# Optimization experiments

Measured on AMD Instinct MI355X. Metric: run time of the kernel, lower is better.

The kernel has to match this reference:

```python
import jax, jax.numpy as jnp
import numpy as np

LN_EPS = 1e-5

def _layer_norm(y, g, b):
    mu = y.mean(-1, keepdims=True)
    var = y.var(-1, keepdims=True)
    return (y - mu) * jax.lax.rsqrt(var + LN_EPS) * g + b

def setup_inputs() -> dict:
    key = jax.random.key(0)
    ks = jax.random.split(key, 10)
    F, D, H = 32, 128, 128
    FD = F * D
    B = 8192
    def rn(k, shape, fan_in):
        return jax.random.normal(k, shape, dtype=jnp.float32) / np.sqrt(fan_in)
    return {
        "x":   jax.random.normal(ks[0], (B, F), dtype=jnp.float32),
        "Wp":  rn(ks[1], (F, D), 1), "bp": jnp.zeros((F, D), jnp.float32),
        "fW1": rn(ks[2], (F, D, H), D), "fb1": jnp.zeros((F, H), jnp.float32),
        "fW2": rn(ks[3], (F, H, D), H), "fb2": jnp.zeros((F, D), jnp.float32),
        "fWg": rn(ks[4], (F, D, 2 * D), D), "fbg": jnp.zeros((F, 2 * D), jnp.float32),
        "fg":  jnp.ones((F, D), jnp.float32), "fbe": jnp.zeros((F, D), jnp.float32),
        "sW1": rn(ks[5], (FD, H), FD), "sb1": jnp.zeros((H,), jnp.float32),
        "sW2": rn(ks[6], (H, FD), H), "sb2": jnp.zeros((FD,), jnp.float32),
        "sWg": rn(ks[7], (FD, 2 * FD), FD), "sbg": jnp.zeros((2 * FD,), jnp.float32),
        "sg":  jnp.ones((FD,), jnp.float32), "sbe": jnp.zeros((FD,), jnp.float32),
        "Wh":  rn(ks[8], (FD, F), FD), "bh": jnp.zeros((F,), jnp.float32),
    }

def reference(x, Wp, bp, fW1, fb1, fW2, fb2, fWg, fbg, fg, fbe,
              sW1, sb1, sW2, sb2, sWg, sbg, sg, sbe, Wh, bh):
    B, F = x.shape
    D = Wp.shape[1]
    # per-feature Linear(1, d_model), batched over all features: (B, F, D)
    emb = x[:, :, None] * Wp[None] + bp[None]
    # per-feature GRNs, batched via einsum over the feature axis
    h = jax.nn.elu(jnp.einsum('bfd,fdh->bfh', emb, fW1) + fb1)
    h = jnp.einsum('bfh,fhd->bfd', h, fW2) + fb2
    gates = jnp.einsum('bfd,fde->bfe', h, fWg) + fbg          # (B, F, 2D)
    a, s = jnp.split(gates, 2, axis=-1)
    stacked = _layer_norm(emb + a * jax.nn.sigmoid(s), fg, fbe)  # (B, F, D)
    # selection GRN over the flattened embeddings
    flat = stacked.reshape(B, F * D)
    hh = jax.nn.elu(flat @ sW1 + sb1)
    hh = hh @ sW2 + sb2
    sgate = flat_gate = hh @ sWg + sbg                          # (B, 2FD)
    sa, ss = jnp.split(sgate, 2, axis=-1)
    sel_in = _layer_norm(flat + sa * jax.nn.sigmoid(ss), sg, sbe)
    weights = jax.nn.softmax(sel_in @ Wh + bh, axis=-1)        # (B, F)
    selected = jnp.einsum('bfd,bf->bd', stacked, weights)      # (B, D)
    return selected, weights
```

## Files before the change

kernel.cpp:

```cpp
#include <hip/hip_runtime.h>
#include <hip/hip_bf16.h>
#include <math.h>

#define BB 8192
#define FF 32
#define DD 128
#define HH 128
#define FD 4096
#define E2 256
#define F2 8192
#define LN_EPS 1e-5f
#define L2E 1.44269504f

typedef __hip_bfloat16 bf16;
typedef __attribute__((ext_vector_type(8))) short bf16x8;
typedef __attribute__((ext_vector_type(4))) float f32x4;

__device__ __forceinline__ float s2f(short s) {
  union { float f; unsigned u; } x; x.u = ((unsigned)(unsigned short)s) << 16; return x.f;
}
__device__ __forceinline__ short f2s(float v) {
  bf16 h = __float2bfloat16(v); return *(short*)&h;
}
__device__ __forceinline__ float fast_sigmoid(float s) {
  return __builtin_amdgcn_rcpf(1.f + __builtin_amdgcn_exp2f(-L2E * s));
}
__device__ __forceinline__ float fast_elu(float v) {
  return v > 0.f ? v : __builtin_amdgcn_exp2f(L2E * v) - 1.f;
}

__device__ __forceinline__ int swz128x64(int row, int hb) {
  return row * 128 + (hb ^ ((row & 7) << 4));
}


__global__ void prep_A1(const float* __restrict__ Wp, const float* __restrict__ bp,
                        const float* __restrict__ fW1, const float* __restrict__ fb1,
                        float* __restrict__ A1, float* __restrict__ C1) {
  int f = blockIdx.x, h = threadIdx.x;
  const float* w1 = fW1 + (size_t)f * DD * HH;
  float a = 0.f, c = 0.f;
  for (int d = 0; d < DD; ++d) {
    float w = w1[d * HH + h];
    a += Wp[f * DD + d] * w;
    c += bp[f * DD + d] * w;
  }
  A1[f * HH + h] = a;
  C1[f * HH + h] = c + fb1[f * HH + h];
}

__global__ void prep_M2(const float* __restrict__ fW2, const float* __restrict__ fWg,
                        float* __restrict__ M2) {
  int f = blockIdx.x, h = blockIdx.y, e = threadIdx.x;
  const float* w2 = fW2 + ((size_t)f * HH + h) * DD;
  const float* wg = fWg + (size_t)f * DD * E2;
  float acc = 0.f;
  for (int d = 0; d < DD; ++d) acc += w2[d] * wg[d * E2 + e];
  M2[((size_t)f * HH + h) * E2 + e] = acc;
}

__global__ void m2_castT(const float* __restrict__ M2, short* __restrict__ M2T) {
  __shared__ float T[64][65];
  int h0 = blockIdx.x * 64, e0 = blockIdx.y * 64, f = blockIdx.z;
  int t = threadIdx.x;
  for (int i = 0; i < 16; ++i) {
    int idx = t + 256 * i; int r = idx >> 6, c = idx & 63;
    T[r][c] = M2[((size_t)f * HH + h0 + r) * E2 + e0 + c];
  }
  __syncthreads();
  for (int i = 0; i < 16; ++i) {
    int idx = t + 256 * i; int e = idx >> 6, h = idx & 63;
    M2T[((size_t)f * E2 + e0 + e) * HH + h0 + h] = f2s(T[h][e]);
  }
}

__global__ void prep_c2(const float* __restrict__ fb2, const float* __restrict__ fWg,
                        const float* __restrict__ fbg, float* __restrict__ c2) {
  int f = blockIdx.x, e = threadIdx.x;
  const float* wg = fWg + (size_t)f * DD * E2;
  float acc = 0.f;
  for (int d = 0; d < DD; ++d) acc += fb2[f * DD + d] * wg[d * E2 + e];
  c2[f * E2 + e] = acc + fbg[f * E2 + e];
}

__global__ void cast_bf16(const float* __restrict__ in, short* __restrict__ out, int n) {
  int i = blockIdx.x * 256 + threadIdx.x;
  if (i < n) out[i] = f2s(in[i]);
}

__global__ void castT(const float* __restrict__ in, short* __restrict__ out, int R, int C) {
  __shared__ float T[64][65];
  int c0 = blockIdx.x * 64, r0 = blockIdx.y * 64;
  int t = threadIdx.x;
  for (int i = 0; i < 16; ++i) {
    int idx = t + 256 * i; int r = idx >> 6, c = idx & 63;
    T[r][c] = in[(size_t)(r0 + r) * C + c0 + c];
  }
  __syncthreads();
  for (int i = 0; i < 16; ++i) {
    int idx = t + 256 * i; int c = idx >> 6, r = idx & 63;
    out[(size_t)(c0 + c) * R + r0 + r] = f2s(T[r][c]);
  }
}

__global__ void init_misc(const float* __restrict__ sbg, const float* __restrict__ bh,
                          float* __restrict__ c3, float* __restrict__ u,
                          float* __restrict__ w0) {
  int j = blockIdx.x * 256 + threadIdx.x;
  c3[j] = sbg[j];
  if (j < 32) { u[j] = 0.f; w0[j] = bh[j]; }
}

__global__ void castT_c3(const float* __restrict__ in, short* __restrict__ out,
                         const float* __restrict__ sb2, float* __restrict__ c3) {
  __shared__ float T[64][65];
  int c0 = blockIdx.x * 64, r0 = blockIdx.y * 64;
  int t = threadIdx.x;
  for (int i = 0; i < 16; ++i) {
    int idx = t + 256 * i; int r = idx >> 6, c = idx & 63;
    T[r][c] = in[(size_t)(r0 + r) * F2 + c0 + c];
  }
  __syncthreads();
  for (int i = 0; i < 16; ++i) {
    int idx = t + 256 * i; int c = idx >> 6, r = idx & 63;
    out[(size_t)(c0 + c) * FD + r0 + r] = f2s(T[r][c]);
  }
  if (t < 64) {
    float s = 0.f;
    for (int r = 0; r < 64; ++r) s += sb2[r0 + r] * T[r][t];
    atomicAdd(&c3[c0 + t], s);
  }
}

__global__ void prep_whs(const float* __restrict__ Wh, const float* __restrict__ sg,
                         const float* __restrict__ sbe, short* __restrict__ WhS,
                         float* __restrict__ u, float* __restrict__ w0) {
  __shared__ float T[64][33];
  int k0 = blockIdx.x * 64;
  int t = threadIdx.x;
  {
    int k = t >> 5, c = t & 31;
    for (int i = 0; i < 8; ++i)
      T[k + 8 * i][c] = Wh[(size_t)(k0 + k + 8 * i) * FF + c];
  }
  __syncthreads();
  {
    int c = t >> 3, kk = (t & 7) * 8;
    short o[8];
    for (int i = 0; i < 8; ++i) o[i] = f2s(sg[k0 + kk + i] * T[kk + i][c]);
    *(bf16x8*)&WhS[(size_t)c * FD + k0 + kk] = *(bf16x8*)&o[0];
  }
  if (t < 32) {
    float su = 0.f, sw = 0.f;
    for (int k = 0; k < 64; ++k) { su += sg[k0 + k] * T[k][t]; sw += sbe[k0 + k] * T[k][t]; }
    atomicAdd(&u[t], su);
    atomicAdd(&w0[t], sw);
  }
}

__global__ __launch_bounds__(256) void gemm_bt_n128_splitk(
    const short* __restrict__ A, const short* __restrict__ BT,
    float* __restrict__ Cp, int M, int K) {
  __shared__ short As[128 * 72];
  __shared__ short Bs[128 * 72];
  int m0 = blockIdx.x * 128;
  int kchunk = K >> 2;
  int kbase = blockIdx.y * kchunk;
  int tid = threadIdx.x;
  int lane = tid & 63, w = tid >> 6;
  int wm = (w >> 1) * 64, wn = (w & 1) * 64;
  int lm = lane & 15, lq = lane >> 4;
  f32x4 acc[4][4] = {};
  for (int kc = 0; kc < kchunk; kc += 64) {
    for (int i = 0; i < 4; ++i) {
      int li = tid + 256 * i;
      int r = li >> 3, c8 = (li & 7) * 8;
      *(bf16x8*)&As[r * 72 + c8] = *(const bf16x8*)&A[(size_t)(m0 + r) * K + kbase + kc + c8];
      *(bf16x8*)&Bs[r * 72 + c8] = *(const bf16x8*)&BT[(size_t)r * K + kbase + kc + c8];
    }
    __syncthreads();
    for (int ks = 0; ks < 2; ++ks) {
      bf16x8 af[4], bfr[4];
      for (int i = 0; i < 4; ++i)
        af[i] = *(const bf16x8*)&As[(wm + i * 16 + lm) * 72 + ks * 32 + lq * 8];
      for (int j = 0; j < 4; ++j)
        bfr[j] = *(const bf16x8*)&Bs[(wn + j * 16 + lm) * 72 + ks * 32 + lq * 8];
      for (int i = 0; i < 4; ++i)
        for (int j = 0; j < 4; ++j)
          acc[i][j] = __builtin_amdgcn_mfma_f32_16x16x32_bf16(af[i], bfr[j], acc[i][j], 0, 0, 0);
    }
    __syncthreads();
  }
  float* out = Cp + (size_t)blockIdx.y * M * 128;
  for (int i = 0; i < 4; ++i)
    for (int j = 0; j < 4; ++j)
      for (int v = 0; v < 4; ++v) {
        int r = wm + i * 16 + lq * 4 + v;
        int c = wn + j * 16 + lm;
        out[(size_t)(m0 + r) * 128 + c] = acc[i][j][v];
      }
}

__global__ void reduce_m3t(const float* __restrict__ Cp, short* __restrict__ M3T, int M) {
  size_t i = (size_t)blockIdx.x * 256 + threadIdx.x;
  float s = 0.f;
  for (int k = 0; k < 4; ++k) s += Cp[(size_t)k * M * 128 + i];
  M3T[i] = f2s(s);
}

__global__ void reduce_hh1(const float* __restrict__ Cp, const float* __restrict__ sb1,
                           short* __restrict__ hh1, int M) {
  size_t i = (size_t)blockIdx.x * 256 + threadIdx.x;
  float s = 0.f;
  for (int k = 0; k < 4; ++k) s += Cp[(size_t)k * M * 128 + i];
  s += sb1[i & 127];
  hh1[i] = f2s(fast_elu(s));
}

__global__ __launch_bounds__(256, 3) void stageA_mfma(
    const float* __restrict__ x, const float* __restrict__ Wp,
    const float* __restrict__ bp, const float* __restrict__ A1,
    const float* __restrict__ C1, const short* __restrict__ M2T,
    const float* __restrict__ c2, const float* __restrict__ fg,
    const float* __restrict__ fbe, short* __restrict__ stacked) {
  __shared__ __align__(16) char SM[3 * 128 * 64 * 2];
  char* As = SM;
  char* Ba = SM + 128 * 64 * 2;
  char* Bb = SM + 2 * 128 * 64 * 2;
  short* Co = (short*)(SM + 128 * 64 * 2);
  float* red = (float*)SM;
  __shared__ float xsh[128];
  int f = blockIdx.y;
  int m0 = blockIdx.x * 128;
  int tid = threadIdx.x;
  int lane = tid & 63, w = tid >> 6;
  int wm = (w >> 1) * 64, wn = (w & 1) * 64;
  int lm = lane & 15, lq = lane >> 4;
  if (tid < 128) xsh[tid] = x[(size_t)(m0 + tid) * FF + f];
  __syncthreads();
  f32x4 accA[4][4] = {}, accB[4][4] = {};
  int c8 = (tid & 7) * 8, rb = tid >> 3;
  for (int kc = 0; kc < HH; kc += 64) {
    {
      f32x4 a1lo = *(const f32x4*)&A1[f * HH + kc + c8];
      f32x4 a1hi = *(const f32x4*)&A1[f * HH + kc + c8 + 4];
      f32x4 c1lo = *(const f32x4*)&C1[f * HH + kc + c8];
      f32x4 c1hi = *(const f32x4*)&C1[f * HH + kc + c8 + 4];
      for (int rr = 0; rr < 4; ++rr) {
        int row = rb + rr * 32;
        float xr = xsh[row];
        short o[8];
        for (int e = 0; e < 4; ++e) {
          o[e]     = f2s(fast_elu(fmaf(xr, a1lo[e], c1lo[e])));
          o[e + 4] = f2s(fast_elu(fmaf(xr, a1hi[e], c1hi[e])));
        }
        *(bf16x8*)(As + swz128x64(row, c8 * 2)) = *(bf16x8*)&o[0];
      }
    }
    for (int i = 0; i < 4; ++i) {
      int li = tid + 256 * i;
      int r = li >> 3, cc = (li & 7) * 8;
      bf16x8 va = *(const bf16x8*)&M2T[((size_t)f * E2 + r) * HH + kc + cc];
      bf16x8 vb = *(const bf16x8*)&M2T[((size_t)f * E2 + 128 + r) * HH + kc + cc];
      *(bf16x8*)(Ba + swz128x64(r, cc * 2)) = va;
      *(bf16x8*)(Bb + swz128x64(r, cc * 2)) = vb;
    }
    __syncthreads();
    for (int ks = 0; ks < 2; ++ks) {
      bf16x8 af[4], ba[4], bb[4];
      int hb = ks * 64 + lq * 16;
      for (int i = 0; i < 4; ++i)
        af[i] = *(const bf16x8*)(As + swz128x64(wm + i * 16 + lm, hb));
      for (int j = 0; j < 4; ++j) {
        ba[j] = *(const bf16x8*)(Ba + swz128x64(wn + j * 16 + lm, hb));
        bb[j] = *(const bf16x8*)(Bb + swz128x64(wn + j * 16 + lm, hb));
      }
      for (int i = 0; i < 4; ++i)
        for (int j = 0; j < 4; ++j) {
          accA[i][j] = __builtin_amdgcn_mfma_f32_16x16x32_bf16(af[i], ba[j], accA[i][j], 0, 0, 0);
          accB[i][j] = __builtin_amdgcn_mfma_f32_16x16x32_bf16(af[i], bb[j], accB[i][j], 0, 0, 0);
        }
    }
    __syncthreads();
  }
  float c2a[4], c2s[4], wpv[4], bpv[4];
  for (int j = 0; j < 4; ++j) {
    int c = wn + j * 16 + lm;
    c2a[j] = c2[f * E2 + c];
    c2s[j] = c2[f * E2 + 128 + c];
    wpv[j] = Wp[f * DD + c];
    bpv[j] = bp[f * DD + c];
  }
  float rs[4][4], rq[4][4];
  for (int i = 0; i < 4; ++i)
    for (int v = 0; v < 4; ++v) {
      int r = wm + i * 16 + lq * 4 + v;
      float xr = xsh[r];
      float sum = 0.f, sq = 0.f;
      for (int j = 0; j < 4; ++j) {
        float a = accA[i][j][v] + c2a[j];
        float s = accB[i][j][v] + c2s[j];
        float emb = fmaf(xr, wpv[j], bpv[j]);
        float y = fmaf(a, fast_sigmoid(s), emb);
        accA[i][j][v] = y;
        sum += y; sq += y * y;
      }
      rs[i][v] = sum; rq[i][v] = sq;
    }
  for (int m = 1; m < 16; m <<= 1)
    for (int i = 0; i < 4; ++i)
      for (int v = 0; v < 4; ++v) {
        rs[i][v] += __shfl_xor(rs[i][v], m, 64);
        rq[i][v] += __shfl_xor(rq[i][v], m, 64);
      }
  if (lm == 0)
    for (int i = 0; i < 4; ++i)
      for (int v = 0; v < 4; ++v) {
        int r = wm + i * 16 + lq * 4 + v;
        red[(w & 1) * 256 + r * 2]     = rs[i][v];
        red[(w & 1) * 256 + r * 2 + 1] = rq[i][v];
      }
  __syncthreads();
  float fgv[4], fbev[4];
  for (int j = 0; j < 4; ++j) {
    int c = wn + j * 16 + lm;
    fgv[j] = fg[f * DD + c];
    fbev[j] = fbe[f * DD + c];
  }
  for (int i = 0; i < 4; ++i)
    for (int v = 0; v < 4; ++v) {
      int r = wm + i * 16 + lq * 4 + v;
      float tot  = red[r * 2]     + red[256 + r * 2];
      float totq = red[r * 2 + 1] + red[256 + r * 2 + 1];
      float mu = tot * (1.f / DD);
      float var = totq * (1.f / DD) - mu * mu;
      float rstd = rsqrtf(var + LN_EPS);
      for (int j = 0; j < 4; ++j) {
        int c = wn + j * 16 + lm;
        Co[r * 128 + c] = f2s((accA[i][j][v] - mu) * rstd * fgv[j] + fbev[j]);
      }
    }
  __syncthreads();
  for (int i = 0; i < 8; ++i) {
    int lin = tid + 256 * i;
    int r = lin >> 4, cc8 = (lin & 15) * 8;
    *(bf16x8*)&stacked[((size_t)(m0 + r) * FF + f) * DD + cc8] = *(bf16x8*)&Co[r * 128 + cc8];
  }
}

__global__ __launch_bounds__(256) void sgate_mfma(
    const short* __restrict__ hh1, const short* __restrict__ M3T,
    const float* __restrict__ c3, const short* __restrict__ stacked,
    short* __restrict__ tmp) {
  __shared__ short As[128 * 72];
  __shared__ short Ba[64 * 72];
  __shared__ short Bb[64 * 72];
  short* Co = As;
  int m0 = blockIdx.x * 128;
  int c0 = blockIdx.y * 64;
  int tid = threadIdx.x;
  int lane = tid & 63, w = tid >> 6;
  int wm = (w >> 1) * 64, wn = (w & 1) * 32;
  int lm = lane & 15, lq = lane >> 4;
  f32x4 accA[4][2] = {}, accB[4][2] = {};
  for (int kc = 0; kc < 128; kc += 64) {
    for (int i = 0; i < 4; ++i) {
      int li = tid + 256 * i;
      int r = li >> 3, c8 = (li & 7) * 8;
      *(bf16x8*)&As[r * 72 + c8] = *(const bf16x8*)&hh1[(size_t)(m0 + r) * 128 + kc + c8];
    }
    for (int i = 0; i < 2; ++i) {
      int li = tid + 256 * i;
      int r = li >> 3, c8 = (li & 7) * 8;
      *(bf16x8*)&Ba[r * 72 + c8] = *(const bf16x8*)&M3T[(size_t)(c0 + r) * 128 + kc + c8];
      *(bf16x8*)&Bb[r * 72 + c8] = *(const bf16x8*)&M3T[(size_t)(4096 + c0 + r) * 128 + kc + c8];
    }
    __syncthreads();
    for (int ks = 0; ks < 2; ++ks) {
      bf16x8 af[4], ba[2], bb[2];
      for (int i = 0; i < 4; ++i)
        af[i] = *(const bf16x8*)&As[(wm + i * 16 + lm) * 72 + ks * 32 + lq * 8];
      for (int j = 0; j < 2; ++j) {
        ba[j] = *(const bf16x8*)&Ba[(wn + j * 16 + lm) * 72 + ks * 32 + lq * 8];
        bb[j] = *(const bf16x8*)&Bb[(wn + j * 16 + lm) * 72 + ks * 32 + lq * 8];
      }
      for (int i = 0; i < 4; ++i)
        for (int j = 0; j < 2; ++j) {
          accA[i][j] = __builtin_amdgcn_mfma_f32_16x16x32_bf16(af[i], ba[j], accA[i][j], 0, 0, 0);
          accB[i][j] = __builtin_amdgcn_mfma_f32_16x16x32_bf16(af[i], bb[j], accB[i][j], 0, 0, 0);
        }
    }
    __syncthreads();
  }
  for (int i = 0; i < 4; ++i)
    for (int j = 0; j < 2; ++j)
      for (int v = 0; v < 4; ++v) {
        int rl = wm + i * 16 + lq * 4 + v;
        int cl = wn + j * 16 + lm;
        int c = c0 + cl;
        float sa = accA[i][j][v] + c3[c];
        float ss = accB[i][j][v] + c3[c + 4096];
        Co[rl * 64 + cl] = f2s(sa * fast_sigmoid(ss));
      }
  __syncthreads();
  for (int i = 0; i < 4; ++i) {
    int lin = tid + 256 * i;
    int r = lin >> 3, c8 = (lin & 7) * 8;
    size_t gi = (size_t)(m0 + r) * FD + c0 + c8;
    bf16x8 sv = *(const bf16x8*)&stacked[gi];
    bf16x8 av = *(bf16x8*)&Co[r * 64 + c8];
    short ov[8];
    for (int e = 0; e < 8; ++e) ov[e] = f2s(s2f(sv[e]) + s2f(av[e]));
    *(bf16x8*)&tmp[gi] = *(bf16x8*)&ov[0];
  }
}

__global__ __launch_bounds__(256) void ln_stats2(const short* __restrict__ tmp,
                                                 float* __restrict__ rowstats) {
  int b = blockIdx.x;
  int t = threadIdx.x;
  const short* row = tmp + (size_t)b * FD;
  bf16x8 v0 = *(const bf16x8*)&row[t * 16];
  bf16x8 v1 = *(const bf16x8*)&row[t * 16 + 8];
  float sum = 0.f, sq = 0.f;
  for (int i = 0; i < 8; ++i) {
    float a = s2f(v0[i]), bv = s2f(v1[i]);
    sum += a + bv; sq += a * a + bv * bv;
  }
  for (int off = 32; off; off >>= 1) { sum += __shfl_down(sum, off); sq += __shfl_down(sq, off); }
  __shared__ float rs[4], rq[4];
  int wid = t >> 6;
  if ((t & 63) == 0) { rs[wid] = sum; rq[wid] = sq; }
  __syncthreads();
  if (t == 0) {
    float tot = rs[0] + rs[1] + rs[2] + rs[3];
    float totq = rq[0] + rq[1] + rq[2] + rq[3];
    float mu = tot * (1.f / FD);
    float var = totq * (1.f / FD) - mu * mu;
    rowstats[2 * b] = mu;
    rowstats[2 * b + 1] = rsqrtf(var + LN_EPS);
  }
}

__global__ __launch_bounds__(256) void gemm_logits_splitk(
    const short* __restrict__ tmp, const short* __restrict__ WhS,
    float* __restrict__ partial) {
  __shared__ short As[128 * 72];
  __shared__ short Bs[32 * 72];
  int m0 = blockIdx.x * 128;
  int kbase = blockIdx.y * (FD / 4);
  int tid = threadIdx.x;
  int lane = tid & 63, w = tid >> 6;
  int wm = w * 32;
  int lm = lane & 15, lq = lane >> 4;
  f32x4 acc[2][2] = {};
  for (int kc = 0; kc < FD / 4; kc += 64) {
    for (int i = 0; i < 4; ++i) {
      int li = tid + 256 * i;
      int r = li >> 3, c8 = (li & 7) * 8;
      *(bf16x8*)&As[r * 72 + c8] = *(const bf16x8*)&tmp[(size_t)(m0 + r) * FD + kbase + kc + c8];
    }
    {
      int r = tid >> 3, c8 = (tid & 7) * 8;
      *(bf16x8*)&Bs[r * 72 + c8] = *(const bf16x8*)&WhS[(size_t)r * FD + kbase + kc + c8];
    }
    __syncthreads();
    for (int ks = 0; ks < 2; ++ks) {
      bf16x8 af[2], bfr[2];
      for (int i = 0; i < 2; ++i)
        af[i] = *(const bf16x8*)&As[(wm + i * 16 + lm) * 72 + ks * 32 + lq * 8];
      for (int j = 0; j < 2; ++j)
        bfr[j] = *(const bf16x8*)&Bs[(j * 16 + lm) * 72 + ks * 32 + lq * 8];
      for (int i = 0; i < 2; ++i)
        for (int j = 0; j < 2; ++j)
          acc[i][j] = __builtin_amdgcn_mfma_f32_16x16x32_bf16(af[i], bfr[j], acc[i][j], 0, 0, 0);
    }
    __syncthreads();
  }
  for (int i = 0; i < 2; ++i)
    for (int j = 0; j < 2; ++j)
      for (int v = 0; v < 4; ++v) {
        int r = m0 + wm + i * 16 + lq * 4 + v;
        int c = j * 16 + lm;
        partial[(size_t)blockIdx.y * BB * FF + (size_t)r * FF + c] = acc[i][j][v];
      }
}

__global__ __launch_bounds__(128) void select_fused(
    const float* __restrict__ partial, const float* __restrict__ rowstats,
    const float* __restrict__ u, const float* __restrict__ w0,
    const short* __restrict__ stacked, float* __restrict__ outsel,
    float* __restrict__ outw) {
  __shared__ float wf[FF];
  __shared__ short L[FD];
  int b = blockIdx.x;
  int t = threadIdx.x;
  for (int i = 0; i < 4; ++i) {
    int idx = t + 128 * i;
    *(bf16x8*)&L[idx * 8] = *(const bf16x8*)&stacked[(size_t)b * FD + idx * 8];
  }
  if (t < 32) {
    float s = 0.f;
    for (int p = 0; p < 4; ++p) s += partial[(size_t)p * BB * FF + (size_t)b * FF + t];
    float mu = rowstats[2 * b], rstd = rowstats[2 * b + 1];
    float l = rstd * s - mu * rstd * u[t] + w0[t];
    float m = l;
    for (int off = 16; off; off >>= 1) m = fmaxf(m, __shfl_xor(m, off, 32));
    float e = __builtin_amdgcn_exp2f(L2E * (l - m));
    float ss = e;
    for (int off = 16; off; off >>= 1) ss += __shfl_xor(ss, off, 32);
    float wv = e / ss;
    wf[t] = wv;
    outw[(size_t)b * FF + t] = wv;
  }
  __syncthreads();
  float acc = 0.f;
  for (int ff = 0; ff < FF; ++ff) acc += s2f(L[ff * 128 + t]) * wf[ff];
  outsel[(size_t)b * DD + t] = acc;
}

extern "C" void kernel_launch(void* const* d_in, const int* in_sizes, int n_in,
                              void* d_out, int out_size, void* d_ws, size_t ws_size,
                              hipStream_t stream) {
  const float* x   = (const float*)d_in[0];
  const float* Wp  = (const float*)d_in[1];
  const float* bp  = (const float*)d_in[2];
  const float* fW1 = (const float*)d_in[3];
  const float* fb1 = (const float*)d_in[4];
  const float* fW2 = (const float*)d_in[5];
  const float* fb2 = (const float*)d_in[6];
  const float* fWg = (const float*)d_in[7];
  const float* fbg = (const float*)d_in[8];
  const float* fg  = (const float*)d_in[9];
  const float* fbe = (const float*)d_in[10];
  const float* sW1 = (const float*)d_in[11];
  const float* sb1 = (const float*)d_in[12];
  const float* sW2 = (const float*)d_in[13];
  const float* sb2 = (const float*)d_in[14];
  const float* sWg = (const float*)d_in[15];
  const float* sbg = (const float*)d_in[16];
  const float* sg  = (const float*)d_in[17];
  const float* sbe = (const float*)d_in[18];
  const float* Wh  = (const float*)d_in[19];
  const float* bh  = (const float*)d_in[20];

  float* w = (float*)d_ws;
  size_t off = 0;
  float* A1   = w + off; off += (size_t)FF * HH;
  float* C1   = w + off; off += (size_t)FF * HH;
  float* c2   = w + off; off += (size_t)FF * E2;
  float* c3   = w + off; off += (size_t)F2;
  float* rowstats = w + off; off += (size_t)2 * BB;
  float* u    = w + off; off += 32;
  float* w0   = w + off; off += 32;
  float* M2   = w + off; off += (size_t)FF * HH * E2;
  float* partial = w + off; off += (size_t)4 * BB * 128;
  short* hh1  = (short*)(w + off); off += (size_t)BB * 128 / 2;
  short* M3T  = (short*)(w + off); off += (size_t)F2 * 128 / 2;
  short* sW2b = (short*)(w + off); off += (size_t)128 * FD / 2;
  short* sW1T = (short*)(w + off); off += (size_t)128 * FD / 2;
  short* M2T  = (short*)(w + off); off += (size_t)FF * E2 * HH / 2;
  short* WhS  = (short*)(w + off); off += (size_t)FF * FD / 2;
  short* stacked = (short*)(w + off); off += (size_t)BB * FD / 2;
  short* tmp  = (short*)(w + off); off += (size_t)BB * FD / 2;
  short* sWgT = (short*)(w + off); off += (size_t)F2 * FD / 2;

  float* outsel = (float*)d_out;
  float* outw   = outsel + (size_t)BB * DD;

  cast_bf16<<<(128 * FD + 255) / 256, 256, 0, stream>>>(sW2, sW2b, 128 * FD);
  castT<<<dim3(DD / 64, FD / 64), 256, 0, stream>>>(sW1, sW1T, FD, DD);
  init_misc<<<F2 / 256, 256, 0, stream>>>(sbg, bh, c3, u, w0);
  castT_c3<<<dim3(F2 / 64, FD / 64), 256, 0, stream>>>(sWg, sWgT, sb2, c3);
  prep_whs<<<FD / 64, 256, 0, stream>>>(Wh, sg, sbe, WhS, u, w0);
  gemm_bt_n128_splitk<<<dim3(F2 / 128, 4), 256, 0, stream>>>(sWgT, sW2b, partial, F2, FD);
  reduce_m3t<<<(F2 * 128) / 256, 256, 0, stream>>>(partial, M3T, F2);
  prep_A1<<<FF, 128, 0, stream>>>(Wp, bp, fW1, fb1, A1, C1);
  prep_M2<<<dim3(FF, HH), E2, 0, stream>>>(fW2, fWg, M2);
  m2_castT<<<dim3(HH / 64, E2 / 64, FF), 256, 0, stream>>>(M2, M2T);
  prep_c2<<<FF, E2, 0, stream>>>(fb2, fWg, fbg, c2);
  stageA_mfma<<<dim3(BB / 128, FF), 256, 0, stream>>>(x, Wp, bp, A1, C1, M2T, c2, fg, fbe,
                                                      stacked);
  gemm_bt_n128_splitk<<<dim3(BB / 128, 4), 256, 0, stream>>>(stacked, sW1T, partial, BB, FD);
  reduce_hh1<<<(BB * 128) / 256, 256, 0, stream>>>(partial, sb1, hh1, BB);
  sgate_mfma<<<dim3(BB / 128, FD / 64), 256, 0, stream>>>(hh1, M3T, c3, stacked, tmp);
  ln_stats2<<<BB, 256, 0, stream>>>(tmp, rowstats);
  gemm_logits_splitk<<<dim3(BB / 128, 4), 256, 0, stream>>>(tmp, WhS, partial);
  select_fused<<<BB, 128, 0, stream>>>(partial, rowstats, u, w0, stacked, outsel, outw);
}
```

Baseline: 589.5 us.

## Fuse LayerNorm row statistics into sgate epilogue via atomics, drop ln_stats2

The sgate kernel epilogue now accumulates per-row sum and sum-of-squares of the bf16 residual output. It reduces them across 8 lanes with shuffles and atomically adds them into rowstats, which init_misc zeroes. select_fused turns the sums into mean and rstd, so the separate ln_stats2 pass that re-read the whole 64MB tmp tensor is removed. This trades a full memory pass for many float atomics per row (64 column blocks per row), with nondeterministic summation order. stageA's MFMA inner loop is also reordered to load the B fragments one j at a time, which lowers register pressure.

```diff
diff --git a/kernel.cpp b/kernel.cpp
--- a/kernel.cpp
+++ b/kernel.cpp
@@ -104,10 +104,12 @@
 }
 
 __global__ void init_misc(const float* __restrict__ sbg, const float* __restrict__ bh,
-                          float* __restrict__ c3, float* __restrict__ u,
-                          float* __restrict__ w0) {
+                          float* __restrict__ c3, float* __restrict__ rowstats,
+                          float* __restrict__ u, float* __restrict__ w0) {
   int j = blockIdx.x * 256 + threadIdx.x;
   c3[j] = sbg[j];
+  rowstats[2 * j] = 0.f;
+  rowstats[2 * j + 1] = 0.f;
   if (j < 32) { u[j] = 0.f; w0[j] = bh[j]; }
 }
 
@@ -267,19 +269,18 @@
     }
     __syncthreads();
     for (int ks = 0; ks < 2; ++ks) {
-      bf16x8 af[4], ba[4], bb[4];
+      bf16x8 af[4];
       int hb = ks * 64 + lq * 16;
       for (int i = 0; i < 4; ++i)
         af[i] = *(const bf16x8*)(As + swz128x64(wm + i * 16 + lm, hb));
       for (int j = 0; j < 4; ++j) {
-        ba[j] = *(const bf16x8*)(Ba + swz128x64(wn + j * 16 + lm, hb));
-        bb[j] = *(const bf16x8*)(Bb + swz128x64(wn + j * 16 + lm, hb));
-      }
-      for (int i = 0; i < 4; ++i)
-        for (int j = 0; j < 4; ++j) {
-          accA[i][j] = __builtin_amdgcn_mfma_f32_16x16x32_bf16(af[i], ba[j], accA[i][j], 0, 0, 0);
-          accB[i][j] = __builtin_amdgcn_mfma_f32_16x16x32_bf16(af[i], bb[j], accB[i][j], 0, 0, 0);
+        bf16x8 ba = *(const bf16x8*)(Ba + swz128x64(wn + j * 16 + lm, hb));
+        bf16x8 bb = *(const bf16x8*)(Bb + swz128x64(wn + j * 16 + lm, hb));
+        for (int i = 0; i < 4; ++i) {
+          accA[i][j] = __builtin_amdgcn_mfma_f32_16x16x32_bf16(af[i], ba, accA[i][j], 0, 0, 0);
+          accB[i][j] = __builtin_amdgcn_mfma_f32_16x16x32_bf16(af[i], bb, accB[i][j], 0, 0, 0);
         }
+      }
     }
     __syncthreads();
   }
@@ -351,7 +352,7 @@
 __global__ __launch_bounds__(256) void sgate_mfma(
     const short* __restrict__ hh1, const short* __restrict__ M3T,
     const float* __restrict__ c3, const short* __restrict__ stacked,
-    short* __restrict__ tmp) {
+    short* __restrict__ tmp, float* __restrict__ rowstats) {
   __shared__ short As[128 * 72];
   __shared__ short Ba[64 * 72];
   __shared__ short Bb[64 * 72];
@@ -410,35 +411,21 @@
     bf16x8 sv = *(const bf16x8*)&stacked[gi];
     bf16x8 av = *(bf16x8*)&Co[r * 64 + c8];
     short ov[8];
-    for (int e = 0; e < 8; ++e) ov[e] = f2s(s2f(sv[e]) + s2f(av[e]));
+    float ps = 0.f, pq = 0.f;
+    for (int e = 0; e < 8; ++e) {
+      short o = f2s(s2f(sv[e]) + s2f(av[e]));
+      ov[e] = o;
+      float vb = s2f(o);
+      ps += vb; pq += vb * vb;
+    }
     *(bf16x8*)&tmp[gi] = *(bf16x8*)&ov[0];
-  }
-}
-
-__global__ __launch_bounds__(256) void ln_stats2(const short* __restrict__ tmp,
-                                                 float* __restrict__ rowstats) {
-  int b = blockIdx.x;
-  int t = threadIdx.x;
-  const short* row = tmp + (size_t)b * FD;
-  bf16x8 v0 = *(const bf16x8*)&row[t * 16];
-  bf16x8 v1 = *(const bf16x8*)&row[t * 16 + 8];
-  float sum = 0.f, sq = 0.f;
-  for (int i = 0; i < 8; ++i) {
-    float a = s2f(v0[i]), bv = s2f(v1[i]);
-    sum += a + bv; sq += a * a + bv * bv;
-  }
-  for (int off = 32; off; off >>= 1) { sum += __shfl_down(sum, off); sq += __shfl_down(sq, off); }
-  __shared__ float rs[4], rq[4];
-  int wid = t >> 6;
-  if ((t & 63) == 0) { rs[wid] = sum; rq[wid] = sq; }
-  __syncthreads();
-  if (t == 0) {
-    float tot = rs[0] + rs[1] + rs[2] + rs[3];
-    float totq = rq[0] + rq[1] + rq[2] + rq[3];
-    float mu = tot * (1.f / FD);
-    float var = totq * (1.f / FD) - mu * mu;
-    rowstats[2 * b] = mu;
-    rowstats[2 * b + 1] = rsqrtf(var + LN_EPS);
+    ps += __shfl_xor(ps, 1, 64); pq += __shfl_xor(pq, 1, 64);
+    ps += __shfl_xor(ps, 2, 64); pq += __shfl_xor(pq, 2, 64);
+    ps += __shfl_xor(ps, 4, 64); pq += __shfl_xor(pq, 4, 64);
+    if ((tid & 7) == 0) {
+      atomicAdd(&rowstats[2 * (m0 + r)], ps);
+      atomicAdd(&rowstats[2 * (m0 + r) + 1], pq);
+    }
   }
 }
 
@@ -502,7 +489,11 @@
   if (t < 32) {
     float s = 0.f;
     for (int p = 0; p < 4; ++p) s += partial[(size_t)p * BB * FF + (size_t)b * FF + t];
-    float mu = rowstats[2 * b], rstd = rowstats[2 * b + 1];
+    float tot  = rowstats[2 * b];
+    float totq = rowstats[2 * b + 1];
+    float mu = tot * (1.f / FD);
+    float var = totq * (1.f / FD) - mu * mu;
+    float rstd = rsqrtf(var + LN_EPS);
     float l = rstd * s - mu * rstd * u[t] + w0[t];
     float m = l;
     for (int off = 16; off; off >>= 1) m = fmaxf(m, __shfl_xor(m, off, 32));
@@ -570,7 +561,7 @@
 
   cast_bf16<<<(128 * FD + 255) / 256, 256, 0, stream>>>(sW2, sW2b, 128 * FD);
   castT<<<dim3(DD / 64, FD / 64), 256, 0, stream>>>(sW1, sW1T, FD, DD);
-  init_misc<<<F2 / 256, 256, 0, stream>>>(sbg, bh, c3, u, w0);
+  init_misc<<<F2 / 256, 256, 0, stream>>>(sbg, bh, c3, rowstats, u, w0);
   castT_c3<<<dim3(F2 / 64, FD / 64), 256, 0, stream>>>(sWg, sWgT, sb2, c3);
   prep_whs<<<FD / 64, 256, 0, stream>>>(Wh, sg, sbe, WhS, u, w0);
   gemm_bt_n128_splitk<<<dim3(F2 / 128, 4), 256, 0, stream>>>(sWgT, sW2b, partial, F2, FD);
@@ -583,8 +574,7 @@
                                                       stacked);
   gemm_bt_n128_splitk<<<dim3(BB / 128, 4), 256, 0, stream>>>(stacked, sW1T, partial, BB, FD);
   reduce_hh1<<<(BB * 128) / 256, 256, 0, stream>>>(partial, sb1, hh1, BB);
-  sgate_mfma<<<dim3(BB / 128, FD / 64), 256, 0, stream>>>(hh1, M3T, c3, stacked, tmp);
-  ln_stats2<<<BB, 256, 0, stream>>>(tmp, rowstats);
+  sgate_mfma<<<dim3(BB / 128, FD / 64), 256, 0, stream>>>(hh1, M3T, c3, stacked, tmp, rowstats);
   gemm_logits_splitk<<<dim3(BB / 128, 4), 256, 0, stream>>>(tmp, WhS, partial);
   select_fused<<<BB, 128, 0, stream>>>(partial, rowstats, u, w0, stacked, outsel, outw);
 }
```

Measured after the change: 594.0 us. About the same (+0.8%).
